# Kernel tuning notes

Measured on AMD Instinct MI355X. Metric: run time of the kernel, lower is better.

The kernel has to match this reference:

```python
import jax, jax.numpy as jnp
import numpy as np

NUM_FEATURE = 512
HIDDEN = 256
NUM_CLASSES = 10
L1 = 1e-4
ALPHA = 1e-3
BATCH = 65536


def setup_inputs() -> dict:
    key = jax.random.key(0)
    k = jax.random.split(key, 6)
    x = jax.random.normal(k[0], (BATCH, NUM_FEATURE), dtype=jnp.float32)
    y = jax.random.randint(k[1], (BATCH,), 0, NUM_CLASSES, dtype=jnp.int32)
    fc0 = jax.random.normal(k[2], (NUM_FEATURE, 512), dtype=jnp.float32) / NUM_FEATURE
    fc1 = jax.random.normal(k[3], (NUM_FEATURE, 512), dtype=jnp.float32) / NUM_FEATURE
    w = jax.random.normal(k[4], (NUM_FEATURE, HIDDEN), dtype=jnp.float32) / NUM_FEATURE
    w1 = jax.random.normal(k[5], (HIDDEN, NUM_CLASSES), dtype=jnp.float32) / HIDDEN
    return {"x": x, "y": y, "fc0": fc0, "fc1": fc1, "w": w, "w1": w1}


def reference(x, y, fc0, fc1, w, w1):
    # sigmoid-gated MLP block with residual
    x1 = x @ fc0                                   # [B, 512]
    x2 = jax.nn.relu(x @ fc1)                      # [B, 512]
    x4 = x + (1.0 + jax.nn.sigmoid(x1)) * x2       # [B, 512] residual

    # head (Dropout(p=0.0) is identity)
    logits = jax.nn.relu(x4 @ w) @ w1              # [B, 10]
    pred = jnp.argmax(logits, axis=1)

    # cross-entropy (mean over batch)
    logp = jax.nn.log_softmax(logits, axis=-1)
    ce = -jnp.mean(jnp.take_along_axis(logp, y[:, None].astype(jnp.int32), axis=1))

    # L1 penalty on all weight matrices
    l1_pen = L1 * (jnp.abs(w1).sum() + jnp.abs(w).sum()
                   + jnp.abs(fc0).sum() + jnp.abs(fc1).sum())

    # per-class variance: sum_i ||mean_{y_i} - x4_i||^2, vectorized via segment sums
    counts = jax.ops.segment_sum(jnp.ones((x4.shape[0],), jnp.float32), y,
                                 num_segments=NUM_CLASSES)
    sums = jax.ops.segment_sum(x4, y, num_segments=NUM_CLASSES)   # [10, 512]
    means = sums / jnp.maximum(counts, 1.0)[:, None]
    var_loss = jnp.sum(jnp.square(means[y] - x4))

    loss = ce + l1_pen + ALPHA * var_loss
    acc = jnp.mean((pred.astype(jnp.int32) == y.astype(jnp.int32)).astype(jnp.float32))
    return (loss, acc)
```

## Files before the change

kernel.cpp:

```cpp
#include <hip/hip_runtime.h>
#include <stdint.h>

#define BATCH 65536
#define FDIM 512
#define HDIM 256
#define NC 10
#define NREP 16

typedef short short8 __attribute__((ext_vector_type(8)));
typedef float f32x4 __attribute__((ext_vector_type(4)));

#define OFF_FC0T   ((size_t)0)
#define OFF_FC1T   (OFF_FC0T + (size_t)512*512*2)
#define OFF_WT     (OFF_FC1T + (size_t)512*512*2)
#define OFF_XT     (OFF_WT   + (size_t)256*512*2)
#define OFF_X4T    (OFF_XT   + (size_t)BATCH*512*2)
#define OFF_ACC    (OFF_X4T  + (size_t)BATCH*512*2)
#define SCAL_SUMSQ 0
#define SCAL_CE    16
#define SCAL_ACC   32
#define SCAL_L1    48
#define SCAL_CTR   64
#define SCAL_N     128
#define CNT_OFF    SCAL_N
#define GSUM_OFF   (SCAL_N + NREP*16)
#define ACC_FLOATS (GSUM_OFF + NREP*5120)
#define OFF_W1T    (OFF_ACC + (size_t)ACC_FLOATS*4)

#define GLL(g,l) __builtin_amdgcn_global_load_lds((const __attribute__((address_space(1))) void*)(g), (__attribute__((address_space(3))) void*)(l), 16, 0, 0)

__device__ __forceinline__ unsigned short f2b(float f){
  unsigned u = __float_as_uint(f);
  u += 0x7FFFu + ((u >> 16) & 1u);
  return (unsigned short)(u >> 16);
}
__device__ __forceinline__ float b2f(unsigned short h){
  return __uint_as_float(((unsigned)h) << 16);
}
__device__ __forceinline__ unsigned pk2b(float f0, float f1){
  unsigned u0 = __float_as_uint(f0) + 0x8000u;
  unsigned u1 = __float_as_uint(f1) + 0x8000u;
  return __builtin_amdgcn_perm(u1, u0, 0x07060302u);
}
__device__ __forceinline__ float ald(const float* p){
  return __hip_atomic_load(p, __ATOMIC_RELAXED, __HIP_MEMORY_SCOPE_AGENT);
}

__global__ __launch_bounds__(256) void k_setup(
    const float* __restrict__ x,   const float* __restrict__ fc0,
    const float* __restrict__ fc1, const float* __restrict__ w,
    const float* __restrict__ w1,  const int* __restrict__ y,
    unsigned short* __restrict__ xT,   unsigned short* __restrict__ fc0T,
    unsigned short* __restrict__ fc1T, unsigned short* __restrict__ wT,
    unsigned short* __restrict__ w1T,  float* __restrict__ accb)
{
  int blk = blockIdx.x, t = threadIdx.x;
  if (blk < 1024){
    __shared__ __align__(16) unsigned short xls[16*520];
    int wv = t >> 6, l = t & 63;
    #pragma unroll 1
    for (int it = 0; it < 4; ++it){
      int I = blk*4 + it;
      #pragma unroll
      for (int rr = 0; rr < 4; ++rr){
        int row = wv*4 + rr;
        const float* src = x + ((size_t)(I*16 + row))*FDIM + l*8;
        float4 v0 = *(const float4*)src;
        float4 v1 = *(const float4*)(src + 4);
        unsigned o[4];
        o[0] = pk2b(v0.x, v0.y); o[1] = pk2b(v0.z, v0.w);
        o[2] = pk2b(v1.x, v1.y); o[3] = pk2b(v1.z, v1.w);
        *(short8*)&xls[row*520 + l*8] = *(short8*)o;
      }
      __syncthreads();
      #pragma unroll
      for (int cc = 0; cc < 4; ++cc){
        int C = cc*4 + wv;
        short8 v = *(const short8*)&xls[(l & 15)*520 + C*32 + (l >> 4)*8];
        *(short8*)&xT[(((size_t)I*16 + C) << 9) + l*8] = v;
      }
      __syncthreads();
    }
    return;
  }
  if (blk < 1360){
    int i = (blk - 1024)*256 + t;
    float l1v = 0.f;
    if (i < 32768){
      int n4 = i&15, m = (i>>4)&3, C = (i>>6)&15, J = i>>10;
      int n = J*16+n4, k8 = C*4+m;
      unsigned short o[8];
      #pragma unroll
      for (int j=0;j<8;++j){ float v = fc0[(size_t)(k8*8+j)*512 + n]; o[j]=f2b(v); l1v += fabsf(v); }
      *(short8*)&fc0T[(size_t)(J*16+C)*512 + (i&63)*8] = *(short8*)o;
    } else if (i < 65536){
      int j0 = i - 32768;
      int n4 = j0&15, m = (j0>>4)&3, C = (j0>>6)&15, J = j0>>10;
      int n = J*16+n4, k8 = C*4+m;
      unsigned short o[8];
      #pragma unroll
      for (int j=0;j<8;++j){ float v = fc1[(size_t)(k8*8+j)*512 + n]; o[j]=f2b(v); l1v += fabsf(v); }
      *(short8*)&fc1T[(size_t)(J*16+C)*512 + (j0&63)*8] = *(short8*)o;
    } else if (i < 81920){
      int j0 = i - 65536;
      int n4 = j0&15, m = (j0>>4)&3, C = (j0>>6)&15, J = j0>>10;
      int n = J*16+n4, k8 = C*4+m;
      unsigned short o[8];
      #pragma unroll
      for (int j=0;j<8;++j){ float v = w[(size_t)(k8*8+j)*256 + n]; o[j]=f2b(v); l1v += fabsf(v); }
      *(short8*)&wT[(size_t)(J*16+C)*512 + (j0&63)*8] = *(short8*)o;
    } else if (i < 86016){
      int j0 = i - 81920;
      int C = j0 >> 9, l = (j0 >> 3) & 63, e = j0 & 7;
      int n = l & 15, k = C*32 + (l>>4)*8 + e;
      float v = (n < NC) ? w1[k*NC + n] : 0.f;
      w1T[C*512 + l*8 + e] = f2b(v);
      if (n < NC) l1v = fabsf(v);
    }
    for (int off = 32; off; off >>= 1) l1v += __shfl_down(l1v, off);
    if ((t & 63) == 0 && l1v != 0.f)
      atomicAdd(&accb[SCAL_L1 + (blk & (NREP-1))], l1v);
    return;
  }
  if (blk < 1441){
    int base = (blk - 1360)*1024;
    #pragma unroll
    for (int j=0;j<4;++j){
      int idx = base + j*256 + t;
      if (idx < ACC_FLOATS && (idx < CNT_OFF || idx >= CNT_OFF + NREP*16))
        accb[idx] = 0.f;
    }
    return;
  }
  {
    __shared__ float cntS[16];
    int b = blk - 1441;
    if (t < 16) cntS[t] = 0.f;
    __syncthreads();
    int base = b*4096;
    for (int i = t; i < 4096; i += 256) atomicAdd(&cntS[y[base+i]], 1.f);
    __syncthreads();
    if (t < 16) accb[CNT_OFF + b*16 + t] = cntS[t];
  }
}


#define BARRIER() __builtin_amdgcn_s_barrier()
#define LGKM0() do{ asm volatile("s_waitcnt lgkmcnt(0)" ::: "memory"); \
                    __builtin_amdgcn_sched_barrier(0); }while(0)

#define RA(AB, C) do{                                                         \
  _Pragma("unroll") for (int m_=0;m_<8;++m_)                                  \
    a[m_] = *(const short8*)((AB) + (((wr*8+m_)*2 + (C))<<10) + lane*16);     \
}while(0)

#define RB(AB, MAT, C) do{                                                    \
  _Pragma("unroll") for (int n_=0;n_<2;++n_)                                  \
    bb[n_] = *(const short8*)((AB) + 32768 + (MAT)*16384 +                    \
                              (((wc*2+n_)*2 + (C))<<10) + lane*16);           \
}while(0)

#define MM16(ACC) do{                                                         \
  __builtin_amdgcn_s_setprio(1);                                              \
  _Pragma("unroll") for (int n_=0;n_<2;++n_)                                  \
  _Pragma("unroll") for (int m_=0;m_<8;++m_)                                  \
    ACC[m_][n_] = __builtin_amdgcn_mfma_f32_16x16x32_bf16(a[m_], bb[n_], ACC[m_][n_], 0,0,0); \
  __builtin_amdgcn_s_setprio(0);                                              \
}while(0)

#define SA(KT, C) do{                                                         \
  char* d_ = ldsd + (((KT)&1) ? 65536 : 0);                                   \
  _Pragma("unroll") for (int r_=0;r_<2;++r_){                                 \
    int I_ = wv + r_*8;                                                       \
    GLL(xb + (((size_t)((rowblk*16 + I_)*16 + (KT)*2 + (C))) << 10) + lane*16,\
        d_ + ((I_*2 + (C)) << 10) + lane*16);                                 \
  } }while(0)

#define SB(KT, C) do{                                                         \
  char* d_ = ldsd + (((KT)&1) ? 65536 : 0) + 32768;                           \
  GLL(b0b + (((size_t)((colblk*8 + wv)*16 + (KT)*2 + (C))) << 10) + lane*16,  \
      d_ + ((wv*2 + (C)) << 10) + lane*16);                                   \
  GLL(b1b + (((size_t)((colblk*8 + wv)*16 + (KT)*2 + (C))) << 10) + lane*16,  \
      d_ + 16384 + ((wv*2 + (C)) << 10) + lane*16);                           \
}while(0)

#define KLOOP() do{                                                           \
  SA(0,0); SB(0,0); SA(0,1); SB(0,1); SA(1,0); SB(1,0); SA(1,1);              \
  asm volatile("s_waitcnt vmcnt(6)" ::: "memory");                            \
  __builtin_amdgcn_sched_barrier(0);                                          \
  BARRIER();                                                                  \
  _Pragma("unroll")                                                           \
  for (int i = 0; i < 4; ++i){                                                \
    int kt0 = 2*i, kt1 = 2*i+1;                                               \
    char* Ab0 = ldsd + ((kt0 & 1) ? 65536 : 0);                               \
    char* Ab1 = ldsd + ((kt1 & 1) ? 65536 : 0);                               \
    RA(Ab0, 0); RB(Ab0, 0, 0);                                                \
    SB(kt1, 1);                                                               \
    BARRIER(); LGKM0(); MM16(acc1);                                           \
    BARRIER();                                                                \
    RB(Ab0, 1, 0);                                                            \
    if (i < 3) SA(kt0+2, 0);                                                  \
    BARRIER(); LGKM0(); MM16(acc2);                                           \
    BARRIER();                                                                \
    RA(Ab0, 1); RB(Ab0, 0, 1);                                                \
    if (i < 3) SB(kt0+2, 0);                                                  \
    BARRIER(); LGKM0(); MM16(acc1);                                           \
    BARRIER();                                                                \
    RB(Ab0, 1, 1);                                                            \
    if (i < 3) SA(kt0+2, 1);                                                  \
    BARRIER(); LGKM0(); MM16(acc2);                                           \
    if (i < 3) { asm volatile("s_waitcnt vmcnt(6)" ::: "memory"); }           \
    else       { asm volatile("s_waitcnt vmcnt(0)" ::: "memory"); }           \
    __builtin_amdgcn_sched_barrier(0);                                        \
    BARRIER();                                                                \
    RA(Ab1, 0); RB(Ab1, 0, 0);                                                \
    if (i < 3) SB(kt0+2, 1);                                                  \
    BARRIER(); LGKM0(); MM16(acc1);                                           \
    BARRIER();                                                                \
    RB(Ab1, 1, 0);                                                            \
    if (i < 3) SA(kt1+2, 0);                                                  \
    BARRIER(); LGKM0(); MM16(acc2);                                           \
    BARRIER();                                                                \
    RA(Ab1, 1); RB(Ab1, 0, 1);                                                \
    if (i < 3) SB(kt1+2, 0);                                                  \
    BARRIER(); LGKM0(); MM16(acc1);                                           \
    BARRIER();                                                                \
    RB(Ab1, 1, 1);                                                            \
    if (i < 3) SA(kt1+2, 1);                                                  \
    BARRIER(); LGKM0(); MM16(acc2);                                           \
    if (i < 3) { asm volatile("s_waitcnt vmcnt(6)" ::: "memory");             \
                 __builtin_amdgcn_sched_barrier(0); }                         \
    BARRIER();                                                                \
  }                                                                           \
}while(0)

__global__ __launch_bounds__(512, 2) void k_gemm12(
    const unsigned short* __restrict__ xT,
    const unsigned short* __restrict__ fc0T,
    const unsigned short* __restrict__ fc1T,
    unsigned short* __restrict__ x4T,
    float* __restrict__ scal)
{
  extern __shared__ __align__(16) char ldsd[];

  int blk = blockIdx.x;
  int wg = (blk & 7)*128 + (blk >> 3);
  int rowblk = wg >> 2;
  int colblk = wg & 3;

  int t = threadIdx.x;
  int wv = t >> 6, lane = t & 63, ln = lane & 15, quad = lane >> 4;
  int wr = wv >> 2, wc = wv & 3;

  const char* xb  = (const char*)xT;
  const char* b0b = (const char*)fc0T;
  const char* b1b = (const char*)fc1T;

  const f32x4 zv = {0.f,0.f,0.f,0.f};
  f32x4 acc1[8][2], acc2[8][2];
  #pragma unroll
  for (int m=0;m<8;++m){ acc1[m][0]=zv; acc1[m][1]=zv; acc2[m][0]=zv; acc2[m][1]=zv; }

  short8 a[8], bb[2];

  KLOOP();

  {
    int Cres = colblk*4 + wc;
    #pragma unroll
    for (int i = 0; i < 8; ++i){
      GLL(xb + (((size_t)((rowblk*16 + wr*8 + i)*16 + Cres)) << 10) + lane*16,
          ldsd + ((wv*8 + i) << 10) + lane*16);
    }
    asm volatile("s_waitcnt vmcnt(0)" ::: "memory");
  }
  __syncthreads();

  unsigned short* resU = (unsigned short*)ldsd;
  unsigned short* x4U  = (unsigned short*)(ldsd + 65536);
  float sumsq = 0.f;
  #pragma unroll
  for (int m = 0; m < 8; ++m){
    #pragma unroll
    for (int n = 0; n < 2; ++n){
      #pragma unroll
      for (int r = 0; r < 4; ++r){
        int slot = (quad*4 + r) | ((n*2 + (ln>>3)) << 4);
        int idx = ((wv*8 + m) << 9) + slot*8 + (ln & 7);
        float xv  = b2f(resU[idx]);
        float x1v = acc1[m][n][r];
        float x2v = fmaxf(acc2[m][n][r], 0.f);
        float gate = 1.f + 1.f/(1.f + __expf(-x1v));
        float x4v = fmaf(gate, x2v, xv);
        unsigned short ub = f2b(x4v);
        float fq = b2f(ub);
        sumsq = fmaf(fq, fq, sumsq);
        x4U[idx] = ub;
      }
    }
  }
  for (int off = 32; off; off >>= 1) sumsq += __shfl_down(sumsq, off);
  __syncthreads();
  float* red = (float*)ldsd;
  if (lane == 0) red[wv] = sumsq;
  __syncthreads();
  if (t == 0){
    float s = 0.f;
    #pragma unroll
    for (int i=0;i<8;++i) s += red[i];
    atomicAdd(&scal[SCAL_SUMSQ + (blk & (NREP-1))], s);
  }
  #pragma unroll
  for (int r = 0; r < 2; ++r){
    int o = r*512 + t;
    int tile = o >> 6, off16 = o & 63;
    int wvp = tile >> 3, i = tile & 7;
    size_t Ig = (size_t)rowblk*16 + (wvp>>2)*8 + i;
    int Cg = colblk*4 + (wvp & 3);
    *(short8*)&x4T[((Ig*16 + Cg) << 9) + off16*8] =
      *(const short8*)&x4U[(tile << 9) + off16*8];
  }
}

__global__ __launch_bounds__(256) void k_csum(const unsigned short* __restrict__ x4T,
                                              const int* __restrict__ y,
                                              float* __restrict__ gsum){
  __shared__ int yS[1024];
  int t = threadIdx.x;
  int wv = t >> 6, l = t & 63;
  int w = blockIdx.x*4 + wv;
  int C = w & 15, Ig = w >> 4;
  int rl = l & 15, q = l >> 4;
  for (int i = t; i < 1024; i += 256) yS[i] = y[Ig*1024 + i];
  __syncthreads();
  float a[NC][8];
  #pragma unroll
  for (int c=0;c<NC;++c)
    #pragma unroll
    for (int e=0;e<8;++e) a[c][e]=0.f;
  for (int ii = 0; ii < 64; ++ii){
    int I = Ig*64 + ii;
    int yv = yS[ii*16 + rl];
    short8 v = *(const short8*)&x4T[(((size_t)I*16 + C) << 9) + l*8];
    float f[8];
    #pragma unroll
    for (int e=0;e<8;++e) f[e] = b2f((unsigned short)v[e]);
    #pragma unroll
    for (int c=0;c<NC;++c){
      bool m = (yv == c);
      #pragma unroll
      for (int e=0;e<8;++e) a[c][e] += m ? f[e] : 0.f;
    }
  }
  #pragma unroll
  for (int off = 1; off < 16; off <<= 1)
    #pragma unroll
    for (int c=0;c<NC;++c)
      #pragma unroll
      for (int e=0;e<8;++e) a[c][e] += __shfl_xor(a[c][e], off);
  if (rl == 0){
    int rep = Ig & (NREP-1);
    int kb = C*32 + q*8;
    #pragma unroll
    for (int c=0;c<NC;++c)
      #pragma unroll
      for (int e=0;e<8;++e)
        atomicAdd(&gsum[(size_t)rep*5120 + c*512 + kb + e], a[c][e]);
  }
}

__global__ __launch_bounds__(512, 2) void k_gemm3_head(
    const unsigned short* __restrict__ x4T,
    const unsigned short* __restrict__ wT,
    const unsigned short* __restrict__ w1T,
    const int* __restrict__ y,
    float* __restrict__ accb,
    float* __restrict__ out)
{
  extern __shared__ __align__(16) char ldsd[];
  __shared__ float redc[8], reda[8];
  __shared__ int lastB;

  float* scal = accb;

  int blk = blockIdx.x;
  int rowblk = blk;
  const int colblk = 0;

  int t = threadIdx.x;
  int wv = t >> 6, lane = t & 63, ln = lane & 15, quad = lane >> 4;
  int wr = wv >> 2, wc = wv & 3;
  int rep = (blk ^ (blk >> 4)) & (NREP-1);

  const char* xb  = (const char*)x4T;
  const char* b0b = (const char*)wT;
  const char* b1b = (const char*)wT + (size_t)128*1024;

  const f32x4 zv = {0.f,0.f,0.f,0.f};
  f32x4 acc1[8][2], acc2[8][2];
  #pragma unroll
  for (int m=0;m<8;++m){ acc1[m][0]=zv; acc1[m][1]=zv; acc2[m][0]=zv; acc2[m][1]=zv; }

  short8 a[8], bb[2];

  KLOOP();

  short8 bw1[8];
  #pragma unroll
  for (int Ck = 0; Ck < 8; ++Ck)
    bw1[Ck] = *(const short8*)&w1T[Ck*512 + lane*8];

  unsigned short* transH = (unsigned short*)ldsd;
  #pragma unroll
  for (int m = 0; m < 8; ++m){
    #pragma unroll
    for (int n = 0; n < 2; ++n){
      #pragma unroll
      for (int r = 0; r < 4; ++r){
        int slot = (quad*4 + r) | ((n*2 + (ln>>3)) << 4);
        int e = ln & 7;
        int IhA = wr*8 + m;
        transH[((IhA*8 + wc)     << 9) + slot*8 + e] = f2b(fmaxf(acc1[m][n][r], 0.f));
        transH[((IhA*8 + 4 + wc) << 9) + slot*8 + e] = f2b(fmaxf(acc2[m][n][r], 0.f));
      }
    }
  }
  __syncthreads();

  f32x4 alog[2] = {zv, zv};
  #pragma unroll
  for (int ih = 0; ih < 2; ++ih){
    int Ih = wv*2 + ih;
    #pragma unroll
    for (int Ck = 0; Ck < 8; ++Ck){
      short8 af = *(const short8*)&transH[((Ih*8 + Ck) << 9) + lane*8];
      alog[ih] = __builtin_amdgcn_mfma_f32_16x16x32_bf16(af, bw1[Ck], alog[ih], 0,0,0);
    }
  }

  float ce_l = 0.f, acc_l = 0.f;
  #pragma unroll
  for (int ih = 0; ih < 2; ++ih){
    #pragma unroll
    for (int r = 0; r < 4; ++r){
      int grow = blk*256 + (wv*2 + ih)*16 + quad*4 + r;
      int yv = y[grow];
      float lg = (ln < NC) ? alog[ih][r] : -1e30f;
      float m = lg; int mi = ln;
      #pragma unroll
      for (int mk = 1; mk < 16; mk <<= 1){
        float om = __shfl_xor(m, mk); int oi = __shfl_xor(mi, mk);
        if (om > m || (om == m && oi < mi)){ m = om; mi = oi; }
      }
      float e  = (ln < NC) ? __expf(lg - m) : 0.f;
      float sy = (ln == yv) ? lg : 0.f;
      #pragma unroll
      for (int mk = 1; mk < 16; mk <<= 1){ e += __shfl_xor(e, mk); sy += __shfl_xor(sy, mk); }
      float lse = m + __logf(e);
      if (ln == 0){ ce_l += (lse - sy); acc_l += (mi == yv) ? 1.f : 0.f; }
    }
  }
  ce_l  += __shfl_down(ce_l, 16);  acc_l += __shfl_down(acc_l, 16);
  ce_l  += __shfl_down(ce_l, 32);  acc_l += __shfl_down(acc_l, 32);
  if (lane == 0){ redc[wv] = ce_l; reda[wv] = acc_l; }
  __syncthreads();
  if (t == 0){
    float c = 0.f, aa = 0.f;
    #pragma unroll
    for (int i=0;i<8;++i){ c += redc[i]; aa += reda[i]; }
    atomicAdd(&scal[SCAL_CE  + rep], c);
    atomicAdd(&scal[SCAL_ACC + rep], aa);
    __threadfence();
    int prev = atomicAdd((int*)(scal + SCAL_CTR), 1);
    lastB = (prev == (int)gridDim.x - 1);
  }
  __syncthreads();
  if (!lastB) return;

  {
    const float* gsum = accb + GSUM_OFF;
    const float* gcnt = accb + CNT_OFF;
    float contrib = 0.f;
    for (int idx = t; idx < 5120; idx += 512){
      float S = 0.f;
      #pragma unroll
      for (int r = 0; r < NREP; ++r) S += ald(&gsum[(size_t)r*5120 + idx]);
      int c = idx >> 9;
      float cnt = 0.f;
      #pragma unroll
      for (int r = 0; r < NREP; ++r) cnt += ald(&gcnt[r*16 + c]);
      contrib += S*S / fmaxf(cnt, 1.f);
    }
    for (int off = 32; off; off >>= 1) contrib += __shfl_down(contrib, off);
    __syncthreads();
    if (lane == 0) redc[wv] = contrib;
    __syncthreads();
    if (t == 0){
      float var2 = 0.f;
      #pragma unroll
      for (int i=0;i<8;++i) var2 += redc[i];
      float sumsq=0.f, ce=0.f, accv=0.f, l1=0.f;
      for (int r=0;r<NREP;++r){
        sumsq += ald(&scal[SCAL_SUMSQ+r]);
        ce    += ald(&scal[SCAL_CE+r]);
        accv  += ald(&scal[SCAL_ACC+r]);
        l1    += ald(&scal[SCAL_L1+r]);
      }
      float var_loss = sumsq - var2;
      out[0] = ce/(float)BATCH + 1e-4f*l1 + 1e-3f*var_loss;
      out[1] = accv/(float)BATCH;
    }
  }
}

extern "C" void kernel_launch(void* const* d_in, const int* in_sizes, int n_in,
                              void* d_out, int out_size, void* d_ws, size_t ws_size,
                              hipStream_t stream){
  (void)in_sizes; (void)n_in; (void)out_size; (void)ws_size;
  const float* x   = (const float*)d_in[0];
  const int*   y   = (const int*)d_in[1];
  const float* fc0 = (const float*)d_in[2];
  const float* fc1 = (const float*)d_in[3];
  const float* w   = (const float*)d_in[4];
  const float* w1  = (const float*)d_in[5];
  char* ws = (char*)d_ws;
  unsigned short* fc0T = (unsigned short*)(ws + OFF_FC0T);
  unsigned short* fc1T = (unsigned short*)(ws + OFF_FC1T);
  unsigned short* wT   = (unsigned short*)(ws + OFF_WT);
  unsigned short* xT   = (unsigned short*)(ws + OFF_XT);
  unsigned short* x4T  = (unsigned short*)(ws + OFF_X4T);
  unsigned short* w1T  = (unsigned short*)(ws + OFF_W1T);
  float* accb = (float*)(ws + OFF_ACC);
  float* scal = accb;
  float* gsum = accb + GSUM_OFF;

  static bool once = [](){
    hipFuncSetAttribute((const void*)k_gemm12,
                        hipFuncAttributeMaxDynamicSharedMemorySize, 131072);
    hipFuncSetAttribute((const void*)k_gemm3_head,
                        hipFuncAttributeMaxDynamicSharedMemorySize, 131072);
    return true;
  }();
  (void)once;

  k_setup<<<1457, 256, 0, stream>>>(x, fc0, fc1, w, w1, y, xT, fc0T, fc1T, wT, w1T, accb);
  k_gemm12<<<1024, 512, 131072, stream>>>(xT, fc0T, fc1T, x4T, scal);
  k_csum<<<256, 256, 0, stream>>>(x4T, y, gsum);
  k_gemm3_head<<<256, 512, 131072, stream>>>(x4T, wT, w1T, y, accb, (float*)d_out);
}
```

Before: 393.2 us.

## Fuse per-class segment sums into gemm12 epilogue and split x transpose blocks

Removes the separate k_csum kernel and computes the per-class column sums of x4 directly in the k_gemm12 epilogue from register-held values. Partial sums are reduced across lanes and waves through LDS and then atomically added to the replicated gsum buffer. This saves a kernel launch and a full re-read of x4T. In exchange it adds epilogue register pressure, extra LDS traffic and more global atomics. Separately, k_setup now processes x with twice as many blocks, each handling half the tiles, for finer-grained parallelism.

After: 354.8 us. 1.11x faster.

```diff
diff --git a/kernel.cpp b/kernel.cpp
--- a/kernel.cpp
+++ b/kernel.cpp
@@ -55,12 +55,12 @@
     unsigned short* __restrict__ w1T,  float* __restrict__ accb)
 {
   int blk = blockIdx.x, t = threadIdx.x;
-  if (blk < 1024){
+  if (blk < 2048){
     __shared__ __align__(16) unsigned short xls[16*520];
     int wv = t >> 6, l = t & 63;
     #pragma unroll 1
-    for (int it = 0; it < 4; ++it){
-      int I = blk*4 + it;
+    for (int it = 0; it < 2; ++it){
+      int I = blk*2 + it;
       #pragma unroll
       for (int rr = 0; rr < 4; ++rr){
         int row = wv*4 + rr;
@@ -83,8 +83,8 @@
     }
     return;
   }
-  if (blk < 1360){
-    int i = (blk - 1024)*256 + t;
+  if (blk < 2384){
+    int i = (blk - 2048)*256 + t;
     float l1v = 0.f;
     if (i < 32768){
       int n4 = i&15, m = (i>>4)&3, C = (i>>6)&15, J = i>>10;
@@ -122,8 +122,8 @@
       atomicAdd(&accb[SCAL_L1 + (blk & (NREP-1))], l1v);
     return;
   }
-  if (blk < 1441){
-    int base = (blk - 1360)*1024;
+  if (blk < 2465){
+    int base = (blk - 2384)*1024;
     #pragma unroll
     for (int j=0;j<4;++j){
       int idx = base + j*256 + t;
@@ -134,7 +134,7 @@
   }
   {
     __shared__ float cntS[16];
-    int b = blk - 1441;
+    int b = blk - 2465;
     if (t < 16) cntS[t] = 0.f;
     __syncthreads();
     int base = b*4096;
@@ -238,10 +238,13 @@
     const unsigned short* __restrict__ xT,
     const unsigned short* __restrict__ fc0T,
     const unsigned short* __restrict__ fc1T,
+    const int* __restrict__ y,
     unsigned short* __restrict__ x4T,
-    float* __restrict__ scal)
+    float* __restrict__ accb)
 {
   extern __shared__ __align__(16) char ldsd[];
+  float* scal = accb;
+  float* gsum = accb + GSUM_OFF;
 
   int blk = blockIdx.x;
   int wg = (blk & 7)*128 + (blk >> 3);
@@ -296,13 +299,53 @@
         float fq = b2f(ub);
         sumsq = fmaf(fq, fq, sumsq);
         x4U[idx] = ub;
+        acc1[m][n][r] = fq;
       }
     }
   }
   for (int off = 32; off; off >>= 1) sumsq += __shfl_down(sumsq, off);
   __syncthreads();
+
+  float cs[NC][2];
+  #pragma unroll
+  for (int c=0;c<NC;++c){ cs[c][0]=0.f; cs[c][1]=0.f; }
+  {
+    const int* yrow = y + rowblk*256 + wr*128;
+    #pragma unroll
+    for (int m = 0; m < 8; ++m){
+      int yv[4];
+      #pragma unroll
+      for (int r = 0; r < 4; ++r) yv[r] = yrow[m*16 + quad*4 + r];
+      #pragma unroll
+      for (int r = 0; r < 4; ++r){
+        float v0 = acc1[m][0][r], v1 = acc1[m][1][r];
+        #pragma unroll
+        for (int c = 0; c < NC; ++c){
+          bool msk = (yv[r] == c);
+          cs[c][0] += msk ? v0 : 0.f;
+          cs[c][1] += msk ? v1 : 0.f;
+        }
+      }
+    }
+  }
+  #pragma unroll
+  for (int c = 0; c < NC; ++c)
+    #pragma unroll
+    for (int n = 0; n < 2; ++n){
+      cs[c][n] += __shfl_xor(cs[c][n], 16);
+      cs[c][n] += __shfl_xor(cs[c][n], 32);
+    }
+
   float* red = (float*)ldsd;
+  float* ct  = (float*)(ldsd + 4096);
   if (lane == 0) red[wv] = sumsq;
+  if (lane < 16){
+    #pragma unroll
+    for (int c = 0; c < NC; ++c)
+      #pragma unroll
+      for (int n = 0; n < 2; ++n)
+        ct[((wv*NC + c)*2 + n)*16 + ln] = cs[c][n];
+  }
   __syncthreads();
   if (t == 0){
     float s = 0.f;
@@ -320,52 +363,12 @@
     *(short8*)&x4T[((Ig*16 + Cg) << 9) + off16*8] =
       *(const short8*)&x4U[(tile << 9) + off16*8];
   }
-}
-
-__global__ __launch_bounds__(256) void k_csum(const unsigned short* __restrict__ x4T,
-                                              const int* __restrict__ y,
-                                              float* __restrict__ gsum){
-  __shared__ int yS[1024];
-  int t = threadIdx.x;
-  int wv = t >> 6, l = t & 63;
-  int w = blockIdx.x*4 + wv;
-  int C = w & 15, Ig = w >> 4;
-  int rl = l & 15, q = l >> 4;
-  for (int i = t; i < 1024; i += 256) yS[i] = y[Ig*1024 + i];
-  __syncthreads();
-  float a[NC][8];
-  #pragma unroll
-  for (int c=0;c<NC;++c)
-    #pragma unroll
-    for (int e=0;e<8;++e) a[c][e]=0.f;
-  for (int ii = 0; ii < 64; ++ii){
-    int I = Ig*64 + ii;
-    int yv = yS[ii*16 + rl];
-    short8 v = *(const short8*)&x4T[(((size_t)I*16 + C) << 9) + l*8];
-    float f[8];
-    #pragma unroll
-    for (int e=0;e<8;++e) f[e] = b2f((unsigned short)v[e]);
-    #pragma unroll
-    for (int c=0;c<NC;++c){
-      bool m = (yv == c);
-      #pragma unroll
-      for (int e=0;e<8;++e) a[c][e] += m ? f[e] : 0.f;
-    }
-  }
-  #pragma unroll
-  for (int off = 1; off < 16; off <<= 1)
-    #pragma unroll
-    for (int c=0;c<NC;++c)
-      #pragma unroll
-      for (int e=0;e<8;++e) a[c][e] += __shfl_xor(a[c][e], off);
-  if (rl == 0){
-    int rep = Ig & (NREP-1);
-    int kb = C*32 + q*8;
-    #pragma unroll
-    for (int c=0;c<NC;++c)
-      #pragma unroll
-      for (int e=0;e<8;++e)
-        atomicAdd(&gsum[(size_t)rep*5120 + c*512 + kb + e], a[c][e]);
+  for (int i = t; i < NC*128; i += 512){
+    int c = i >> 7, col = i & 127;
+    int wcx = col >> 5, nx = (col >> 4) & 1, lnx = col & 15;
+    float v = ct[((wcx*NC + c)*2 + nx)*16 + lnx]
+            + ct[(((4+wcx)*NC + c)*2 + nx)*16 + lnx];
+    atomicAdd(&gsum[(size_t)(blk & (NREP-1))*5120 + c*512 + colblk*128 + col], v);
   }
 }
 
@@ -531,8 +534,6 @@
   unsigned short* x4T  = (unsigned short*)(ws + OFF_X4T);
   unsigned short* w1T  = (unsigned short*)(ws + OFF_W1T);
   float* accb = (float*)(ws + OFF_ACC);
-  float* scal = accb;
-  float* gsum = accb + GSUM_OFF;
 
   static bool once = [](){
     hipFuncSetAttribute((const void*)k_gemm12,
@@ -543,8 +544,7 @@
   }();
   (void)once;
 
-  k_setup<<<1457, 256, 0, stream>>>(x, fc0, fc1, w, w1, y, xT, fc0T, fc1T, wT, w1T, accb);
-  k_gemm12<<<1024, 512, 131072, stream>>>(xT, fc0T, fc1T, x4T, scal);
-  k_csum<<<256, 256, 0, stream>>>(x4T, y, gsum);
+  k_setup<<<2481, 256, 0, stream>>>(x, fc0, fc1, w, w1, y, xT, fc0T, fc1T, wT, w1T, accb);
+  k_gemm12<<<1024, 512, 131072, stream>>>(xT, fc0T, fc1T, y, x4T, accb);
   k_gemm3_head<<<256, 512, 131072, stream>>>(x4T, wT, w1T, y, accb, (float*)d_out);
 }
```
